# Kernel tuning notes

Measured on AMD Instinct MI355X. Metric: run time of the kernel, lower is better.

Reference implementation:

```python
import jax, jax.numpy as jnp
import numpy as np

D_MODEL = 1024
NUM_HEADS = 16
HEAD_DIM = D_MODEL // NUM_HEADS
B, T = 2, 2048


def setup_inputs() -> dict:
    key = jax.random.key(0)
    kx, kq, kk, kv, ko = jax.random.split(key, 5)
    s = 1.0 / np.sqrt(D_MODEL)  # ~Linear init scale
    return {
        "x": jax.random.normal(kx, (B, T, D_MODEL), dtype=jnp.float32),
        "Wq": jax.random.normal(kq, (D_MODEL, D_MODEL), dtype=jnp.float32) * s,
        "Wk": jax.random.normal(kk, (D_MODEL, D_MODEL), dtype=jnp.float32) * s,
        "Wv": jax.random.normal(kv, (D_MODEL, D_MODEL), dtype=jnp.float32) * s,
        "Wo": jax.random.normal(ko, (D_MODEL, D_MODEL), dtype=jnp.float32) * s,
    }


def reference(x, Wq, Wk, Wv, Wo):
    Bc, Tc, _ = x.shape
    H, D = NUM_HEADS, HEAD_DIM
    scale = jnp.sqrt(jnp.asarray(D, x.dtype))
    # torch Linear (bias=False): y = x @ W^T
    q = (x @ Wq.T).reshape(Bc, Tc, H, D).transpose(0, 2, 1, 3)  # [B,H,T,D]
    k = (x @ Wk.T).reshape(Bc, Tc, H, D).transpose(0, 2, 1, 3)
    v = (x @ Wv.T).reshape(Bc, Tc, H, D).transpose(0, 2, 1, 3)
    scores = jnp.einsum("bhtd,bhsd->bhts", q, k) / scale  # [B,H,T,T]
    # causal bias: upper triangle (strictly future positions) gets -1e9
    causal_bias = jnp.triu(jnp.ones((Tc, Tc), dtype=jnp.float32), k=1) * -1e9
    scores = scores + causal_bias
    weights = jax.nn.softmax(scores, axis=-1)
    # dropout is identity in eval / p=0
    out = jnp.einsum("bhts,bhsd->bhtd", weights, v)  # [B,H,T,D]
    out = out.transpose(0, 2, 1, 3).reshape(Bc, Tc, H * D)
    return out @ Wo.T
```

## Files before the change

kernel.cpp:

```cpp
#include <hip/hip_runtime.h>
#include <hip/hip_bf16.h>

typedef __bf16 bf16_t;
typedef __bf16 bf16x2 __attribute__((ext_vector_type(2)));
typedef __bf16 bf16x4 __attribute__((ext_vector_type(4)));
typedef __bf16 bf16x8 __attribute__((ext_vector_type(8)));
typedef float  f32x4  __attribute__((ext_vector_type(4)));
typedef int    i32x2  __attribute__((ext_vector_type(2)));

#define D_MODEL 1024
#define HEADS   16
#define HD      64
#define BB      2
#define TT      2048
#define MROWS   (BB*TT)

#define GLDS16(g, l) __builtin_amdgcn_global_load_lds( \
    (const __attribute__((address_space(1))) void*)(g), \
    (__attribute__((address_space(3))) void*)(l), 16, 0, 0)

static __device__ __forceinline__ int pack_bf16(float a, float b) {
    bf16x2 t; t[0] = (bf16_t)a; t[1] = (bf16_t)b;
    return __builtin_bit_cast(int, t);
}

__global__ __launch_bounds__(256) void cvt_all_kernel(const float* __restrict__ x,
                                                      const float* __restrict__ wq,
                                                      const float* __restrict__ wk,
                                                      const float* __restrict__ wv,
                                                      const float* __restrict__ wo,
                                                      bf16_t* __restrict__ dst) {
    const int i = blockIdx.x * 256 + threadIdx.x;
    const float* src;
    int s;
    if (i < 1048576) { src = x; s = i; }
    else {
        int j = i - 1048576;
        int w = j >> 18;
        s = j & 262143;
        src = (w == 0) ? wq : (w == 1) ? wk : (w == 2) ? wv : wo;
    }
    float4 v = reinterpret_cast<const float4*>(src)[s];
    bf16x4 o;
    o[0] = (bf16_t)v.x; o[1] = (bf16_t)v.y; o[2] = (bf16_t)v.z; o[3] = (bf16_t)v.w;
    reinterpret_cast<bf16x4*>(dst)[i] = o;
}

template<int MODE, int BN>
__global__ __launch_bounds__(256) void gemm_bt(const bf16_t* __restrict__ A,
                                               const bf16_t* __restrict__ Bw,
                                               void* __restrict__ Cout,
                                               int M, int N, int K) {
    constexpr int NI = BN / 32;
    __shared__ __align__(16) bf16_t As[128*32];
    __shared__ __align__(16) bf16_t Bs[BN*32];
    const int tid   = threadIdx.x;
    const int lane  = tid & 63;
    const int wave  = tid >> 6;
    const int col16 = lane & 15;
    const int quad  = lane >> 4;
    const int wrow  = (wave & 1) * 64;
    const int wcol  = (wave >> 1) * (BN / 2);
    const int bm    = blockIdx.y * 128;
    const int bn    = blockIdx.x * BN;

    const int lr = tid >> 2;
    const int lc = (tid & 3) * 8;

    const bf16_t* agp = &A [(size_t)(bm + lr)*K + lc];
    const bf16_t* bgp = &Bw[(size_t)(bn + lr)*K + lc];
    const size_t half = (size_t)64 * K;
    bf16_t* as_lo = &As[wave*512];
    bf16_t* as_hi = &As[2048 + wave*512];
    bf16_t* bs_lo = &Bs[wave*512];
    bf16_t* bs_hi = &Bs[2048 + wave*512];

    f32x4 acc[4][NI];
#pragma unroll
    for (int i = 0; i < 4; i++)
#pragma unroll
        for (int j = 0; j < NI; j++) acc[i][j] = (f32x4){0.f, 0.f, 0.f, 0.f};

    for (int k0 = 0; k0 < K; k0 += 32) {
        GLDS16(agp + k0,        as_lo);
        GLDS16(agp + half + k0, as_hi);
        GLDS16(bgp + k0,        bs_lo);
        if (BN == 128) GLDS16(bgp + half + k0, bs_hi);
        __syncthreads();

        bf16x8 af[4], bfr[NI];
#pragma unroll
        for (int mi = 0; mi < 4; mi++)
            af[mi] = *reinterpret_cast<const bf16x8*>(&As[(wrow + mi*16 + col16)*32 + quad*8]);
#pragma unroll
        for (int ni = 0; ni < NI; ni++)
            bfr[ni] = *reinterpret_cast<const bf16x8*>(&Bs[(wcol + ni*16 + col16)*32 + quad*8]);
#pragma unroll
        for (int mi = 0; mi < 4; mi++)
#pragma unroll
            for (int ni = 0; ni < NI; ni++)
                acc[mi][ni] = __builtin_amdgcn_mfma_f32_16x16x32_bf16(af[mi], bfr[ni], acc[mi][ni], 0, 0, 0);
        __syncthreads();
    }

#pragma unroll
    for (int mi = 0; mi < 4; mi++) {
#pragma unroll
        for (int r = 0; r < 4; r++) {
            const int gm = bm + wrow + mi*16 + quad*4 + r;
            const int t  = gm & (TT - 1);
            const int b  = gm >> 11;
#pragma unroll
            for (int ni = 0; ni < NI; ni++) {
                const int gn = bn + wcol + ni*16 + col16;
                float v = acc[mi][ni][r];
                if (MODE == 2) {
                    reinterpret_cast<float*>(Cout)[(size_t)gm * N + gn] = v;
                } else {
                    const int which = gn >> 10;
                    if (which == 0) v *= 0.18033688f;
                    const int n = gn & 1023;
                    const int h = n >> 6, d = n & 63;
                    const size_t off = (size_t)(which == 2 ? 3 : which) * MROWS * D_MODEL;
                    bf16_t* base = reinterpret_cast<bf16_t*>(Cout) + off;
                    base[(((size_t)(b*HEADS + h))*TT + t)*HD + d] = (bf16_t)v;
                }
            }
        }
    }
}

__global__ __launch_bounds__(256) void transpose_v(const bf16_t* __restrict__ V,
                                                   bf16_t* __restrict__ Vt) {
    __shared__ bf16_t tile[64][72];
    const int tid = threadIdx.x;
    const int bh = blockIdx.y;
    const int t0 = blockIdx.x * 64;
    const bf16_t* src = V + ((size_t)bh * TT + t0) * HD;
#pragma unroll
    for (int i = 0; i < 2; i++) {
        const int r = i*32 + (tid >> 3), c = (tid & 7) * 8;
        *reinterpret_cast<bf16x8*>(&tile[r][c]) =
            *reinterpret_cast<const bf16x8*>(&src[(size_t)r * HD + c]);
    }
    __syncthreads();
    bf16_t* dst = Vt + (size_t)bh * HD * TT + t0;
#pragma unroll
    for (int i = 0; i < 2; i++) {
        const int d = i*32 + (tid >> 3), tc = (tid & 7) * 8;
        bf16x8 o;
#pragma unroll
        for (int j = 0; j < 8; j++) o[j] = tile[tc + j][d];
        *reinterpret_cast<bf16x8*>(&dst[(size_t)d * TT + tc]) = o;
    }
}

__global__ __launch_bounds__(256, 4) void attn_kernel(const bf16_t* __restrict__ Q,
                                                      const bf16_t* __restrict__ Kk,
                                                      const bf16_t* __restrict__ Vt,
                                                      bf16_t* __restrict__ O) {
    __shared__ __align__(16) bf16_t Ks[2][64*64];
    __shared__ __align__(16) bf16_t Vs[2][64*64];

    const int tid   = threadIdx.x;
    const int lane  = tid & 63;
    const int wave  = tid >> 6;
    const int col16 = lane & 15;
    const int quad  = lane >> 4;
    const int kw    = wave & 1;
    const int qw    = wave >> 1;

    const int bx = blockIdx.x;
    const int r_ = bx >> 8, s_ = bx & 255;
    const int bh = s_ & 31;
    const int g  = s_ >> 5;
    const int qt = (r_ == 0) ? (31 - g)
                 : (r_ == 1) ? g
                 : (r_ == 2) ? (15 - g)
                             : (16 + g);
    const int qb    = qt * 64;
    const int qbase = qb + qw * 32;
    const int nkt   = qt + 1;

    const bf16_t* Qb = Q  + (size_t)bh * TT * HD;
    const bf16_t* Kb = Kk + (size_t)bh * TT * HD;
    const bf16_t* Vb = Vt + (size_t)bh * HD * TT;

    bf16x8 qf[2][2];
#pragma unroll
    for (int qg = 0; qg < 2; qg++)
#pragma unroll
        for (int h = 0; h < 2; h++)
            qf[qg][h] = *reinterpret_cast<const bf16x8*>(
                &Qb[(size_t)(qbase + qg*16 + col16)*HD + h*32 + quad*8]);

    const int srow = (tid >> 3) & 31;
    const int sg   = ((lane & 7) ^ (srow & 7)) * 8;

    auto stage = [&](int kt, int buf) {
        const int s0 = kt * 64;
        GLDS16(&Kb[(size_t)(s0 + srow)*HD + sg],        &Ks[buf][wave*512]);
        GLDS16(&Kb[(size_t)(s0 + srow + 32)*HD + sg],   &Ks[buf][2048 + wave*512]);
        GLDS16(&Vb[(size_t)srow*TT + s0 + sg],          &Vs[buf][wave*512]);
        GLDS16(&Vb[(size_t)(srow + 32)*TT + s0 + sg],   &Vs[buf][2048 + wave*512]);
    };

    f32x4 acc[4][2];
#pragma unroll
    for (int i = 0; i < 4; i++)
#pragma unroll
        for (int j = 0; j < 2; j++) acc[i][j] = (f32x4){0.f,0.f,0.f,0.f};
    float lsum[2] = {0.f, 0.f};

    const int x7 = col16 & 7;
#if !__has_builtin(__builtin_amdgcn_permlane32_swap)
    const int a1 = ((quad & 1) * 32 + col16) * 4;
    const int a2 = a1 + 64;
    const bool hi = quad >= 2;
#endif

    stage(0, 0);
    __syncthreads();

    for (int kt = 0; kt < nkt; kt++) {
        const int buf = kt & 1;
        if (kt + 1 < nkt) stage(kt + 1, buf ^ 1);
        const int s0 = kt * 64;
        const bool diag = (kt == nkt - 1);

        bf16x8 k0[2], k1[2];
#pragma unroll
        for (int c = 0; c < 2; c++) {
            k0[c] = *reinterpret_cast<const bf16x8*>(
                &Ks[buf][(kw*32 + c*16 + col16)*64 + ((0*4 + quad) ^ x7)*8]);
            k1[c] = *reinterpret_cast<const bf16x8*>(
                &Ks[buf][(kw*32 + c*16 + col16)*64 + ((1*4 + quad) ^ x7)*8]);
        }

        int pk[2][2][2];
#pragma unroll
        for (int c = 0; c < 2; c++) {
#pragma unroll
            for (int qg = 0; qg < 2; qg++) {
                f32x4 sv = __builtin_amdgcn_mfma_f32_16x16x32_bf16(k0[c], qf[qg][0], (f32x4){0.f,0.f,0.f,0.f}, 0, 0, 0);
                sv       = __builtin_amdgcn_mfma_f32_16x16x32_bf16(k1[c], qf[qg][1], sv, 0, 0, 0);

                float pr[4];
#pragma unroll
                for (int r = 0; r < 4; r++) pr[r] = exp2f(sv[r]);
                if (diag) {
#pragma unroll
                    for (int r = 0; r < 4; r++)
                        if (s0 + kw*32 + c*16 + quad*4 + r > qbase + qg*16 + col16) pr[r] = 0.f;
                }
                lsum[qg] += (pr[0] + pr[1]) + (pr[2] + pr[3]);
                pk[c][qg][0] = pack_bf16(pr[0], pr[1]);
                pk[c][qg][1] = pack_bf16(pr[2], pr[3]);
            }
        }

        bf16x8 pf[2];
#pragma unroll
        for (int qg = 0; qg < 2; qg++) {
#if __has_builtin(__builtin_amdgcn_permlane32_swap)
            i32x2 u0 = __builtin_amdgcn_permlane32_swap(pk[0][qg][0], pk[1][qg][0], false, false);
            i32x2 v0 = __builtin_amdgcn_permlane16_swap(u0[0], u0[1], false, false);
            i32x2 u1 = __builtin_amdgcn_permlane32_swap(pk[0][qg][1], pk[1][qg][1], false, false);
            i32x2 v1 = __builtin_amdgcn_permlane16_swap(u1[0], u1[1], false, false);
            int4 bi = { v0[0], v1[0], v0[1], v1[1] };
#else
            int b0l = __builtin_amdgcn_ds_bpermute(a1, pk[0][qg][0]);
            int b0h = __builtin_amdgcn_ds_bpermute(a1, pk[1][qg][0]);
            int b1l = __builtin_amdgcn_ds_bpermute(a1, pk[0][qg][1]);
            int b1h = __builtin_amdgcn_ds_bpermute(a1, pk[1][qg][1]);
            int b2l = __builtin_amdgcn_ds_bpermute(a2, pk[0][qg][0]);
            int b2h = __builtin_amdgcn_ds_bpermute(a2, pk[1][qg][0]);
            int b3l = __builtin_amdgcn_ds_bpermute(a2, pk[0][qg][1]);
            int b3h = __builtin_amdgcn_ds_bpermute(a2, pk[1][qg][1]);
            int4 bi = { hi ? b0h : b0l, hi ? b1h : b1l, hi ? b2h : b2l, hi ? b3h : b3l };
#endif
            pf[qg] = __builtin_bit_cast(bf16x8, bi);
        }
#pragma unroll
        for (int c = 0; c < 4; c++) {
            bf16x8 vf = *reinterpret_cast<const bf16x8*>(
                &Vs[buf][(c*16 + col16)*64 + ((kw*4 + quad) ^ x7)*8]);
            acc[c][0] = __builtin_amdgcn_mfma_f32_16x16x32_bf16(vf, pf[0], acc[c][0], 0, 0, 0);
            acc[c][1] = __builtin_amdgcn_mfma_f32_16x16x32_bf16(vf, pf[1], acc[c][1], 0, 0, 0);
        }
        __syncthreads();
    }

#pragma unroll
    for (int qg = 0; qg < 2; qg++) {
        lsum[qg] += __shfl_xor(lsum[qg], 16);
        lsum[qg] += __shfl_xor(lsum[qg], 32);
    }

    float* Mq = qw ? reinterpret_cast<float*>(&Vs[0][0])
                   : reinterpret_cast<float*>(&Ks[0][0]);
    float* LS = reinterpret_cast<float*>(&Vs[0][0]) + 32*68;

    if (kw == 1) {
#pragma unroll
        for (int c = 0; c < 4; c++)
#pragma unroll
            for (int qg = 0; qg < 2; qg++)
                *reinterpret_cast<f32x4*>(&Mq[(qg*16 + col16)*68 + c*16 + quad*4]) = acc[c][qg];
        if (lane < 16) {
            LS[qw*32 + lane]      = lsum[0];
            LS[qw*32 + 16 + lane] = lsum[1];
        }
    }
    __syncthreads();

    if (kw == 0) {
        const int b_ = bh >> 4, h = bh & 15;
#pragma unroll
        for (int qg = 0; qg < 2; qg++) {
            const float l   = lsum[qg] + LS[qw*32 + qg*16 + col16];
            const float inv = 1.0f / l;
            const int t = qbase + qg*16 + col16;
            bf16_t* Ob = &O[(((size_t)(b_*TT + t))*HEADS + h)*HD + quad*4];
#pragma unroll
            for (int c = 0; c < 4; c++) {
                f32x4 m = *reinterpret_cast<const f32x4*>(&Mq[(qg*16 + col16)*68 + c*16 + quad*4]);
                bf16x4 o4;
#pragma unroll
                for (int r = 0; r < 4; r++) o4[r] = (bf16_t)((acc[c][qg][r] + m[r]) * inv);
                *reinterpret_cast<bf16x4*>(&Ob[c*16]) = o4;
            }
        }
    }
}

extern "C" void kernel_launch(void* const* d_in, const int* in_sizes, int n_in,
                              void* d_out, int out_size, void* d_ws, size_t ws_size,
                              hipStream_t stream) {
    const float* x  = (const float*)d_in[0];
    const float* Wq = (const float*)d_in[1];
    const float* Wk = (const float*)d_in[2];
    const float* Wv = (const float*)d_in[3];
    const float* Wo = (const float*)d_in[4];
    float* out = (float*)d_out;

    bf16_t* Xb  = (bf16_t*)d_ws;
    bf16_t* Wqb = Xb  + (size_t)MROWS * D_MODEL;
    bf16_t* Wob = Wqb + (size_t)3 * D_MODEL * D_MODEL;
    bf16_t* Qw  = Wob + (size_t)D_MODEL * D_MODEL;
    bf16_t* Kw  = Qw  + (size_t)MROWS * D_MODEL;
    bf16_t* Vt  = Kw  + (size_t)MROWS * D_MODEL;
    bf16_t* Ow  = Vt  + (size_t)MROWS * D_MODEL;

    cvt_all_kernel<<<(MROWS*D_MODEL + 4*D_MODEL*D_MODEL) / 4 / 256, 256, 0, stream>>>(
        x, Wq, Wk, Wv, Wo, Xb);

    dim3 gqkv(3 * D_MODEL / 128, MROWS / 128);
    gemm_bt<0,128><<<gqkv, 256, 0, stream>>>(Xb, Wqb, Qw, MROWS, 3 * D_MODEL, D_MODEL);

    dim3 gt(TT / 64, BB * HEADS);
    transpose_v<<<gt, 256, 0, stream>>>(Ow, Vt);

    attn_kernel<<<dim3(1024), 256, 0, stream>>>(Qw, Kw, Vt, Ow);

    dim3 go(D_MODEL / 64, MROWS / 128);
    gemm_bt<2,64><<<go, 256, 0, stream>>>(Ow, Wob, out, MROWS, D_MODEL, D_MODEL);
}
```

Before: 187.4 us.

## Split long causal query tiles across two blocks with atomic-counter merge

```diff
diff --git a/kernel.cpp b/kernel.cpp
--- a/kernel.cpp
+++ b/kernel.cpp
@@ -24,12 +24,45 @@
     return __builtin_bit_cast(int, t);
 }
 
+__constant__ unsigned char TQT[8][5] = {
+    {23, 22, 31,  1,  0},
+    {21, 20, 31,  3,  2},
+    {19, 18, 30,  5,  4},
+    {17, 16, 15,  7,  6},
+    {14, 28, 13, 12,  8},
+    {29, 29, 27, 11,  9},
+    {30, 27, 24, 25, 10},
+    {28, 26, 25, 26, 24},
+};
+__constant__ unsigned char TK0[8][5] = {
+    { 0,  0,  0,  0,  0},
+    { 0,  0, 16,  0,  0},
+    { 0,  0,  0,  0,  0},
+    { 0,  0,  0,  0,  0},
+    { 0,  0,  0,  0,  0},
+    { 0, 15,  0,  0,  0},
+    {16, 14,  0,  0,  0},
+    {15,  0, 13, 14, 13},
+};
+__constant__ unsigned char TK1[8][5] = {
+    {24, 23, 16,  2,  1},
+    {22, 21, 32,  4,  3},
+    {20, 19, 16,  6,  5},
+    {18, 17, 16,  8,  7},
+    {15, 15, 14, 13,  9},
+    {15, 30, 14, 12, 10},
+    {31, 28, 13, 13, 11},
+    {29, 14, 26, 27, 25},
+};
+
 __global__ __launch_bounds__(256) void cvt_all_kernel(const float* __restrict__ x,
                                                       const float* __restrict__ wq,
                                                       const float* __restrict__ wk,
                                                       const float* __restrict__ wv,
                                                       const float* __restrict__ wo,
-                                                      bf16_t* __restrict__ dst) {
+                                                      bf16_t* __restrict__ dst,
+                                                      unsigned int* __restrict__ cnt) {
+    if (blockIdx.x == 0) cnt[threadIdx.x] = 0;
     const int i = blockIdx.x * 256 + threadIdx.x;
     const float* src;
     int s;
@@ -155,10 +188,13 @@
     }
 }
 
-__global__ __launch_bounds__(256, 4) void attn_kernel(const bf16_t* __restrict__ Q,
+__global__ __launch_bounds__(256, 5) void attn_kernel(const bf16_t* __restrict__ Q,
                                                       const bf16_t* __restrict__ Kk,
                                                       const bf16_t* __restrict__ Vt,
-                                                      bf16_t* __restrict__ O) {
+                                                      bf16_t* __restrict__ O,
+                                                      float* __restrict__ Opart,
+                                                      float* __restrict__ Lpart,
+                                                      unsigned int* __restrict__ cnt) {
     __shared__ __align__(16) bf16_t Ks[2][64*64];
     __shared__ __align__(16) bf16_t Vs[2][64*64];
 
@@ -174,13 +210,12 @@
     const int r_ = bx >> 8, s_ = bx & 255;
     const int bh = s_ & 31;
     const int g  = s_ >> 5;
-    const int qt = (r_ == 0) ? (31 - g)
-                 : (r_ == 1) ? g
-                 : (r_ == 2) ? (15 - g)
-                             : (16 + g);
+    const int qt = TQT[g][r_];
+    const int k0 = TK0[g][r_];
+    const int k1 = TK1[g][r_];
+    const bool split = (qt >= 24);
     const int qb    = qt * 64;
     const int qbase = qb + qw * 32;
-    const int nkt   = qt + 1;
 
     const bf16_t* Qb = Q  + (size_t)bh * TT * HD;
     const bf16_t* Kb = Kk + (size_t)bh * TT * HD;
@@ -213,27 +248,22 @@
     float lsum[2] = {0.f, 0.f};
 
     const int x7 = col16 & 7;
-#if !__has_builtin(__builtin_amdgcn_permlane32_swap)
-    const int a1 = ((quad & 1) * 32 + col16) * 4;
-    const int a2 = a1 + 64;
-    const bool hi = quad >= 2;
-#endif
-
-    stage(0, 0);
+
+    stage(k0, 0);
     __syncthreads();
 
-    for (int kt = 0; kt < nkt; kt++) {
-        const int buf = kt & 1;
-        if (kt + 1 < nkt) stage(kt + 1, buf ^ 1);
+    int buf = 0;
+    for (int kt = k0; kt < k1; kt++) {
+        if (kt + 1 < k1) stage(kt + 1, buf ^ 1);
         const int s0 = kt * 64;
-        const bool diag = (kt == nkt - 1);
-
-        bf16x8 k0[2], k1[2];
+        const bool diag = (kt == qt);
+
+        bf16x8 kf0[2], kf1[2];
 #pragma unroll
         for (int c = 0; c < 2; c++) {
-            k0[c] = *reinterpret_cast<const bf16x8*>(
+            kf0[c] = *reinterpret_cast<const bf16x8*>(
                 &Ks[buf][(kw*32 + c*16 + col16)*64 + ((0*4 + quad) ^ x7)*8]);
-            k1[c] = *reinterpret_cast<const bf16x8*>(
+            kf1[c] = *reinterpret_cast<const bf16x8*>(
                 &Ks[buf][(kw*32 + c*16 + col16)*64 + ((1*4 + quad) ^ x7)*8]);
         }
 
@@ -242,8 +272,8 @@
         for (int c = 0; c < 2; c++) {
 #pragma unroll
             for (int qg = 0; qg < 2; qg++) {
-                f32x4 sv = __builtin_amdgcn_mfma_f32_16x16x32_bf16(k0[c], qf[qg][0], (f32x4){0.f,0.f,0.f,0.f}, 0, 0, 0);
-                sv       = __builtin_amdgcn_mfma_f32_16x16x32_bf16(k1[c], qf[qg][1], sv, 0, 0, 0);
+                f32x4 sv = __builtin_amdgcn_mfma_f32_16x16x32_bf16(kf0[c], qf[qg][0], (f32x4){0.f,0.f,0.f,0.f}, 0, 0, 0);
+                sv       = __builtin_amdgcn_mfma_f32_16x16x32_bf16(kf1[c], qf[qg][1], sv, 0, 0, 0);
 
                 float pr[4];
 #pragma unroll
@@ -269,6 +299,9 @@
             i32x2 v1 = __builtin_amdgcn_permlane16_swap(u1[0], u1[1], false, false);
             int4 bi = { v0[0], v1[0], v0[1], v1[1] };
 #else
+            const int a1 = ((quad & 1) * 32 + col16) * 4;
+            const int a2 = a1 + 64;
+            const bool hi = quad >= 2;
             int b0l = __builtin_amdgcn_ds_bpermute(a1, pk[0][qg][0]);
             int b0h = __builtin_amdgcn_ds_bpermute(a1, pk[1][qg][0]);
             int b1l = __builtin_amdgcn_ds_bpermute(a1, pk[0][qg][1]);
@@ -288,6 +321,7 @@
             acc[c][0] = __builtin_amdgcn_mfma_f32_16x16x32_bf16(vf, pf[0], acc[c][0], 0, 0, 0);
             acc[c][1] = __builtin_amdgcn_mfma_f32_16x16x32_bf16(vf, pf[1], acc[c][1], 0, 0, 0);
         }
+        buf ^= 1;
         __syncthreads();
     }
 
@@ -314,21 +348,75 @@
     }
     __syncthreads();
 
+    const int b_ = bh >> 4, h = bh & 15;
+    const int p  = bh * 8 + (qt - 24);
     if (kw == 0) {
-        const int b_ = bh >> 4, h = bh & 15;
+        const int half = (k0 == 0) ? 0 : 1;
+        float* Op = Opart + ((size_t)p * 2 + half) * 4096;
+        float* Lp = Lpart + ((size_t)p * 2 + half) * 64;
 #pragma unroll
         for (int qg = 0; qg < 2; qg++) {
-            const float l   = lsum[qg] + LS[qw*32 + qg*16 + col16];
+            const float l  = lsum[qg] + LS[qw*32 + qg*16 + col16];
+            const int   ql = qw*32 + qg*16 + col16;
+            if (!split) {
+                const float inv = 1.0f / l;
+                const int t = qb + ql;
+                bf16_t* Ob = &O[(((size_t)(b_*TT + t))*HEADS + h)*HD + quad*4];
+#pragma unroll
+                for (int c = 0; c < 4; c++) {
+                    f32x4 m = *reinterpret_cast<const f32x4*>(&Mq[(qg*16 + col16)*68 + c*16 + quad*4]);
+                    bf16x4 o4;
+#pragma unroll
+                    for (int r = 0; r < 4; r++) o4[r] = (bf16_t)((acc[c][qg][r] + m[r]) * inv);
+                    *reinterpret_cast<bf16x4*>(&Ob[c*16]) = o4;
+                }
+            } else {
+                if (quad == 0)
+                    __hip_atomic_store(&Lp[ql], l, __ATOMIC_RELAXED, __HIP_MEMORY_SCOPE_AGENT);
+#pragma unroll
+                for (int c = 0; c < 4; c++) {
+                    f32x4 m = *reinterpret_cast<const f32x4*>(&Mq[(qg*16 + col16)*68 + c*16 + quad*4]);
+#pragma unroll
+                    for (int r = 0; r < 4; r++)
+                        __hip_atomic_store(&Op[ql*64 + c*16 + quad*4 + r], acc[c][qg][r] + m[r],
+                                           __ATOMIC_RELAXED, __HIP_MEMORY_SCOPE_AGENT);
+                }
+            }
+        }
+    }
+
+    if (split) {
+        int* wf = reinterpret_cast<int*>(reinterpret_cast<char*>(&Ks[0][0]) + 12288);
+        __syncthreads();
+        if (tid == 0) {
+            unsigned int old = __hip_atomic_fetch_add(&cnt[p], 1u, __ATOMIC_ACQ_REL,
+                                                      __HIP_MEMORY_SCOPE_AGENT);
+            *wf = (old == 1);
+        }
+        __syncthreads();
+        if (*wf) {
+            const float* O0 = Opart + (size_t)p * 2 * 4096;
+            const float* O1 = O0 + 4096;
+            const float* L0 = Lpart + (size_t)p * 2 * 64;
+            const float* L1 = L0 + 64;
+            const int q  = tid >> 2;
+            const int d0 = (tid & 3) * 16;
+            const float l = __hip_atomic_load(&L0[q], __ATOMIC_RELAXED, __HIP_MEMORY_SCOPE_AGENT)
+                          + __hip_atomic_load(&L1[q], __ATOMIC_RELAXED, __HIP_MEMORY_SCOPE_AGENT);
             const float inv = 1.0f / l;
-            const int t = qbase + qg*16 + col16;
-            bf16_t* Ob = &O[(((size_t)(b_*TT + t))*HEADS + h)*HD + quad*4];
-#pragma unroll
-            for (int c = 0; c < 4; c++) {
-                f32x4 m = *reinterpret_cast<const f32x4*>(&Mq[(qg*16 + col16)*68 + c*16 + quad*4]);
+            const int t = qb + q;
+            bf16_t* Ob = &O[(((size_t)(b_*TT + t))*HEADS + h)*HD + d0];
+#pragma unroll
+            for (int j = 0; j < 16; j += 4) {
                 bf16x4 o4;
 #pragma unroll
-                for (int r = 0; r < 4; r++) o4[r] = (bf16_t)((acc[c][qg][r] + m[r]) * inv);
-                *reinterpret_cast<bf16x4*>(&Ob[c*16]) = o4;
+                for (int rr = 0; rr < 4; rr++) {
+                    const int idx = q*64 + d0 + j + rr;
+                    float a = __hip_atomic_load(&O0[idx], __ATOMIC_RELAXED, __HIP_MEMORY_SCOPE_AGENT)
+                            + __hip_atomic_load(&O1[idx], __ATOMIC_RELAXED, __HIP_MEMORY_SCOPE_AGENT);
+                    o4[rr] = (bf16_t)(a * inv);
+                }
+                *reinterpret_cast<bf16x4*>(&Ob[j]) = o4;
             }
         }
     }
@@ -351,9 +439,12 @@
     bf16_t* Kw  = Qw  + (size_t)MROWS * D_MODEL;
     bf16_t* Vt  = Kw  + (size_t)MROWS * D_MODEL;
     bf16_t* Ow  = Vt  + (size_t)MROWS * D_MODEL;
+    float*        Opart = (float*)Xb;
+    unsigned int* cnt   = (unsigned int*)((char*)d_ws + (size_t)48*1024*1024);
+    float*        Lpart = (float*)((char*)d_ws + (size_t)48*1024*1024 + 1024);
 
     cvt_all_kernel<<<(MROWS*D_MODEL + 4*D_MODEL*D_MODEL) / 4 / 256, 256, 0, stream>>>(
-        x, Wq, Wk, Wv, Wo, Xb);
+        x, Wq, Wk, Wv, Wo, Xb, cnt);
 
     dim3 gqkv(3 * D_MODEL / 128, MROWS / 128);
     gemm_bt<0,128><<<gqkv, 256, 0, stream>>>(Xb, Wqb, Qw, MROWS, 3 * D_MODEL, D_MODEL);
@@ -361,7 +452,7 @@
     dim3 gt(TT / 64, BB * HEADS);
     transpose_v<<<gt, 256, 0, stream>>>(Ow, Vt);
 
-    attn_kernel<<<dim3(1024), 256, 0, stream>>>(Qw, Kw, Vt, Ow);
+    attn_kernel<<<dim3(1280), 256, 0, stream>>>(Qw, Kw, Vt, Ow, Opart, Lpart, cnt);
 
     dim3 go(D_MODEL / 64, MROWS / 128);
     gemm_bt<2,64><<<go, 256, 0, stream>>>(Ow, Wob, out, MROWS, D_MODEL, D_MODEL);
```

After: 226.9 us. +21.1%, slower.
